# Kernel optimization log

Measured on AMD Instinct MI355X. Metric: run time of the kernel, lower is better.

Reference implementation:

```python
import jax, jax.numpy as jnp
import numpy as np

H = 4
D = 64          # attention_head_size
HID = H * D     # 256
LN_EPS = 1e-12


def setup_inputs() -> dict:
    key = jax.random.key(0)
    ks = jax.random.split(key, 20)
    B, S = 8, 200
    s = 0.02
    inp = {
        'input_tensor': jax.random.normal(ks[0], (B, S, HID), jnp.float32),
        'attention_mask': jnp.zeros((B, 1, S, S), jnp.float32),
        'absolute_pos_K': jax.random.normal(ks[1], (B, S, HID), jnp.float32),
        'absolute_pos_V': jax.random.normal(ks[2], (B, S, HID), jnp.float32),
        'time_matrix_emb_K': jax.random.normal(ks[3], (B, S, S, HID), jnp.float32),
        'time_matrix_emb_V': jax.random.normal(ks[4], (B, S, S, HID), jnp.float32),
        'Wq': jax.random.normal(ks[5], (HID, HID), jnp.float32) * s,
        'bq': jnp.zeros((HID,), jnp.float32),
        'Wk': jax.random.normal(ks[6], (HID, HID), jnp.float32) * s,
        'bk': jnp.zeros((HID,), jnp.float32),
        'Wv': jax.random.normal(ks[7], (HID, HID), jnp.float32) * s,
        'bv': jnp.zeros((HID,), jnp.float32),
        'order_w': jax.random.normal(ks[8], (2 * D,), jnp.float32) * s,
        'order_b': jnp.zeros((), jnp.float32),
        'dist_w': jax.random.normal(ks[9], (2 * D,), jnp.float32) * s,
        'dist_b': jnp.zeros((), jnp.float32),
        'scalar': jax.random.normal(ks[10], (1,), jnp.float32),
        'Wd': jax.random.normal(ks[11], (HID, HID), jnp.float32) * s,
        'bd': jnp.zeros((HID,), jnp.float32),
        'ln_g': jnp.ones((HID,), jnp.float32),
        'ln_b': jnp.zeros((HID,), jnp.float32),
    }
    return inp


def _forward(input_tensor, attention_mask, absolute_pos_K, absolute_pos_V,
             time_matrix_emb_K, time_matrix_emb_V,
             Wq, bq, Wk, bk, Wv, bv, order_w, order_b, dist_w, dist_b,
             scalar, Wd, bd, ln_g, ln_b):
    B, S, _ = input_tensor.shape
    heads = lambda x: x.reshape(B, S, H, D).transpose(0, 2, 1, 3)  # -> [B,H,S,D]
    q = heads(input_tensor @ Wq + bq)
    k = heads(input_tensor @ Wk + bk)
    v = heads(input_tensor @ Wv + bv)
    posK = heads(absolute_pos_K)                                   # [B,H,S,D]
    posV = heads(absolute_pos_V)
    timeK = time_matrix_emb_K.reshape(B, S, S, H, D).transpose(0, 3, 1, 2, 4)  # [B,H,S,S,D]
    timeV = time_matrix_emb_V.reshape(B, S, S, H, D).transpose(0, 3, 1, 2, 4)

    scores = (jnp.einsum('bhid,bhjd->bhij', q, k)
              + jnp.einsum('bhid,bhjd->bhij', q, posK)
              + jnp.einsum('bhijd,bhid->bhij', timeK, q))          # [B,H,S,S]

    # order_affine(cat(q_i,k_j)) == q_i@w[:D] + k_j@w[D:] + b (Linear on concat)
    pr_order = jax.nn.sigmoid(jnp.einsum('bhid,d->bhi', q, order_w[:D])[:, :, :, None]
                              + jnp.einsum('bhjd,d->bhj', k, order_w[D:])[:, :, None, :]
                              + order_b)
    gd_order = jnp.triu(jnp.ones((S, S), jnp.float32), 1)[None, None]
    error_order = (jnp.log(pr_order + 1e-24) * gd_order
                   + jnp.log(1.0 - pr_order + 1e-24) * (1.0 - gd_order))

    idx = jnp.arange(S, dtype=jnp.float32)
    gd_dist = jnp.log(jnp.abs(idx[None, :] - idx[:, None]) + 1.0)[None, None]
    pr_dist = (jnp.einsum('bhid,d->bhi', q, dist_w[:D])[:, :, :, None]
               + jnp.einsum('bhjd,d->bhj', k, dist_w[D:])[:, :, None, :]
               + dist_b)
    error_distance = -jnp.square(gd_dist - pr_dist) * jnp.square(scalar[0]) / 2.0

    scores = scores + error_order + error_distance
    probs = jax.nn.softmax(scores / np.sqrt(D) + attention_mask, axis=-1)

    ctx = (jnp.einsum('bhij,bhjd->bhid', probs, v)
           + jnp.einsum('bhij,bhjd->bhid', probs, posV)
           + jnp.einsum('bhij,bhijd->bhid', probs, timeV))
    ctx = ctx.transpose(0, 2, 1, 3).reshape(B, S, HID)

    hs = ctx @ Wd + bd + input_tensor
    mu = jnp.mean(hs, axis=-1, keepdims=True)
    var = jnp.mean(jnp.square(hs - mu), axis=-1, keepdims=True)
    return (hs - mu) / jnp.sqrt(var + LN_EPS) * ln_g + ln_b


def reference(input_tensor, attention_mask, absolute_pos_K, absolute_pos_V,
              time_matrix_emb_K, time_matrix_emb_V,
              Wq, bq, Wk, bk, Wv, bv, order_w, order_b, dist_w, dist_b,
              scalar, Wd, bd, ln_g, ln_b):
    return _forward(input_tensor, attention_mask, absolute_pos_K, absolute_pos_V,
                    time_matrix_emb_K, time_matrix_emb_V,
                    Wq, bq, Wk, bk, Wv, bv, order_w, order_b, dist_w, dist_b,
                    scalar, Wd, bd, ln_g, ln_b)
```

## Files before the change

kernel.cpp:

```cpp
#include <hip/hip_runtime.h>

#define SB 8
#define SS 200
#define HID 256
#define NH 4
#define DH 64

typedef float f32x4_t __attribute__((ext_vector_type(4)));

__device__ __forceinline__ float4 ntload4(const float* p) {
    f32x4_t v = __builtin_nontemporal_load((const f32x4_t*)p);
    return make_float4(v.x, v.y, v.z, v.w);
}

__global__ __launch_bounds__(256) void proj_fused_kernel(
    const float* __restrict__ in,
    const float* __restrict__ Wq, const float* __restrict__ bq,
    const float* __restrict__ Wk, const float* __restrict__ bk,
    const float* __restrict__ Wv, const float* __restrict__ bv,
    const float* __restrict__ posK, const float* __restrict__ posV,
    const float* __restrict__ order_w, const float* __restrict__ dist_w,
    float* __restrict__ q_out, float* __restrict__ kpk_out,
    float* __restrict__ vpv_out,
    float* __restrict__ qo, float* __restrict__ ko,
    float* __restrict__ qd, float* __restrict__ kd)
{
    const int which = blockIdx.y;
    const float* W = (which == 0) ? Wq : (which == 1) ? Wk : Wv;
    const float* bias = (which == 0) ? bq : (which == 1) ? bk : bv;
    const int row0 = blockIdx.x * 8;
    __shared__ float sin_[8][HID];
    const int t = threadIdx.x;
    #pragma unroll
    for (int r = 0; r < 8; r++)
        sin_[r][t] = in[(size_t)(row0 + r) * HID + t];
    __syncthreads();

    const int tx = t & 63, ty = t >> 6;
    const int c0 = tx * 4, r0 = ty * 2;
    float acc[2][4] = {};
    #pragma unroll 4
    for (int kk = 0; kk < HID; kk++) {
        const float4 wv4 = *(const float4*)(W + (size_t)kk * HID + c0);
        const float a0 = sin_[r0][kk];
        const float a1 = sin_[r0 + 1][kk];
        acc[0][0] += a0 * wv4.x; acc[0][1] += a0 * wv4.y;
        acc[0][2] += a0 * wv4.z; acc[0][3] += a0 * wv4.w;
        acc[1][0] += a1 * wv4.x; acc[1][1] += a1 * wv4.y;
        acc[1][2] += a1 * wv4.z; acc[1][3] += a1 * wv4.w;
    }

    const float4 b4 = *(const float4*)(bias + c0);
    const int hh = tx >> 4;
    const int dd4 = (tx & 15) * 4;
    float4 ow4 = make_float4(0.f, 0.f, 0.f, 0.f);
    float4 dw4 = make_float4(0.f, 0.f, 0.f, 0.f);
    if (which == 0) {
        ow4 = *(const float4*)(order_w + dd4);
        dw4 = *(const float4*)(dist_w + dd4);
    } else if (which == 1) {
        ow4 = *(const float4*)(order_w + 64 + dd4);
        dw4 = *(const float4*)(dist_w + 64 + dd4);
    }

    #pragma unroll
    for (int rr = 0; rr < 2; rr++) {
        const int row = row0 + r0 + rr;
        const size_t off = (size_t)row * HID + c0;
        float4 o;
        o.x = acc[rr][0] + b4.x;
        o.y = acc[rr][1] + b4.y;
        o.z = acc[rr][2] + b4.z;
        o.w = acc[rr][3] + b4.w;
        if (which == 0) {
            *(float4*)(q_out + off) = o;
            float po = o.x * ow4.x + o.y * ow4.y + o.z * ow4.z + o.w * ow4.w;
            float pd = o.x * dw4.x + o.y * dw4.y + o.z * dw4.z + o.w * dw4.w;
            #pragma unroll
            for (int m = 1; m <= 8; m <<= 1) {
                po += __shfl_xor(po, m, 64);
                pd += __shfl_xor(pd, m, 64);
            }
            if ((tx & 15) == 0) {
                qo[row * NH + hh] = po;
                qd[row * NH + hh] = pd;
            }
        } else if (which == 1) {
            const float4 p4 = *(const float4*)(posK + off);
            float4 s;
            s.x = o.x + p4.x; s.y = o.y + p4.y;
            s.z = o.z + p4.z; s.w = o.w + p4.w;
            *(float4*)(kpk_out + off) = s;
            float po = o.x * ow4.x + o.y * ow4.y + o.z * ow4.z + o.w * ow4.w;
            float pd = o.x * dw4.x + o.y * dw4.y + o.z * dw4.z + o.w * dw4.w;
            #pragma unroll
            for (int m = 1; m <= 8; m <<= 1) {
                po += __shfl_xor(po, m, 64);
                pd += __shfl_xor(pd, m, 64);
            }
            if ((tx & 15) == 0) {
                ko[row * NH + hh] = po;
                kd[row * NH + hh] = pd;
            }
        } else {
            const float4 p4 = *(const float4*)(posV + off);
            float4 s;
            s.x = o.x + p4.x; s.y = o.y + p4.y;
            s.z = o.z + p4.z; s.w = o.w + p4.w;
            *(float4*)(vpv_out + off) = s;
        }
    }
}

__global__ __launch_bounds__(256) void attn_fused_kernel(
    const float* __restrict__ q, const float* __restrict__ kpk,
    const float* __restrict__ vpv,
    const float* __restrict__ timeK, const float* __restrict__ timeV,
    const float* __restrict__ mask,
    const float* __restrict__ qo, const float* __restrict__ ko,
    const float* __restrict__ qd, const float* __restrict__ kd,
    const float* __restrict__ order_b_p, const float* __restrict__ dist_b_p,
    const float* __restrict__ scalar_p,
    const float* __restrict__ Wd, const float* __restrict__ bd,
    const float* __restrict__ input,
    const float* __restrict__ ln_g, const float* __restrict__ ln_b,
    float* __restrict__ out)
{
    const int blk = blockIdx.x;
    const int b = blk / SS, i = blk - b * SS;
    const int t = threadIdx.x;
    const int w = t >> 6, l = t & 63;
    const int h = l >> 4;
    const int sub = l & 15;

    __shared__ float sh_q[HID];
    __shared__ float sh_e[NH][SS + 8];
    __shared__ float sh_s[NH][SS + 8];
    __shared__ float sh_red[4][HID];
    __shared__ float sh_c[HID];
    __shared__ float red2[4];

    const size_t rowq = (size_t)blk * HID;
    sh_q[t] = q[rowq + t];

    const float order_b = *order_b_p;
    const float dist_b = *dist_b_p;
    const float sc = *scalar_p;
    const float sc2h = 0.5f * sc * sc;
    const size_t tb = (size_t)blk * SS;
    for (int idx = t; idx < NH * SS; idx += 256) {
        const int eh = idx & 3, j = idx >> 2;
        const float xo = qo[blk * NH + eh] + ko[(b * SS + j) * NH + eh] + order_b;
        const float pr = 1.0f / (1.0f + __expf(-xo));
        const float eo = (j > i) ? __logf(pr + 1e-24f) : __logf(1.0f - pr + 1e-24f);
        const float xd = qd[blk * NH + eh] + kd[(b * SS + j) * NH + eh] + dist_b;
        const float gd = __logf(fabsf((float)(i - j)) + 1.0f);
        const float dv = gd - xd;
        sh_e[eh][j] = (eo - dv * dv * sc2h) * 0.125f + mask[tb + j];
    }
    __syncthreads();

    const int d0 = l * 4;
    const float4 qr = *(const float4*)(sh_q + d0);

    for (int j0 = 0; j0 < SS; j0 += 8) {
        const int ja = j0 + w, jb = ja + 4;
        const float4 ta = ntload4(timeK + (tb + ja) * (size_t)HID + d0);
        const float4 tb4 = ntload4(timeK + (tb + jb) * (size_t)HID + d0);
        const float4 ka = *(const float4*)(kpk + ((size_t)(b * SS + ja)) * HID + d0);
        const float4 kb = *(const float4*)(kpk + ((size_t)(b * SS + jb)) * HID + d0);
        float pa = (ta.x + ka.x) * qr.x + (ta.y + ka.y) * qr.y
                 + (ta.z + ka.z) * qr.z + (ta.w + ka.w) * qr.w;
        float pb = (tb4.x + kb.x) * qr.x + (tb4.y + kb.y) * qr.y
                 + (tb4.z + kb.z) * qr.z + (tb4.w + kb.w) * qr.w;
        pa += __shfl_xor(pa, 1, 64); pb += __shfl_xor(pb, 1, 64);
        pa += __shfl_xor(pa, 2, 64); pb += __shfl_xor(pb, 2, 64);
        pa += __shfl_xor(pa, 4, 64); pb += __shfl_xor(pb, 4, 64);
        pa += __shfl_xor(pa, 8, 64); pb += __shfl_xor(pb, 8, 64);
        if (sub == 0) {
            sh_s[h][ja] = pa * 0.125f + sh_e[h][ja];
            sh_s[h][jb] = pb * 0.125f + sh_e[h][jb];
        }
    }
    __syncthreads();

    {
        float vals[4];
        float m = -1e30f;
        #pragma unroll
        for (int rep = 0; rep < 4; rep++) {
            const int j = l + rep * 64;
            vals[rep] = (j < SS) ? sh_s[w][j] : -1e30f;
            m = fmaxf(m, vals[rep]);
        }
        #pragma unroll
        for (int mm = 32; mm >= 1; mm >>= 1) m = fmaxf(m, __shfl_xor(m, mm, 64));
        float sum = 0.0f;
        float es[4];
        #pragma unroll
        for (int rep = 0; rep < 4; rep++) {
            const int j = l + rep * 64;
            if (j < SS) { es[rep] = __expf(vals[rep] - m); sum += es[rep]; }
        }
        #pragma unroll
        for (int mm = 32; mm >= 1; mm >>= 1) sum += __shfl_xor(sum, mm, 64);
        const float inv = 1.0f / sum;
        #pragma unroll
        for (int rep = 0; rep < 4; rep++) {
            const int j = l + rep * 64;
            if (j < SS) sh_s[w][j] = es[rep] * inv;
        }
    }
    __syncthreads();

    float4 acc = make_float4(0.f, 0.f, 0.f, 0.f);
    for (int j0 = 0; j0 < SS; j0 += 8) {
        const int ja = j0 + w, jb = ja + 4;
        const float4 ta = ntload4(timeV + (tb + ja) * (size_t)HID + d0);
        const float4 tb4 = ntload4(timeV + (tb + jb) * (size_t)HID + d0);
        const float4 va = *(const float4*)(vpv + ((size_t)(b * SS + ja)) * HID + d0);
        const float4 vb = *(const float4*)(vpv + ((size_t)(b * SS + jb)) * HID + d0);
        const float pa = sh_s[h][ja];
        const float pb = sh_s[h][jb];
        acc.x += pa * (ta.x + va.x) + pb * (tb4.x + vb.x);
        acc.y += pa * (ta.y + va.y) + pb * (tb4.y + vb.y);
        acc.z += pa * (ta.z + va.z) + pb * (tb4.z + vb.z);
        acc.w += pa * (ta.w + va.w) + pb * (tb4.w + vb.w);
    }
    *(float4*)(&sh_red[w][d0]) = acc;
    __syncthreads();
    sh_c[t] = sh_red[0][t] + sh_red[1][t] + sh_red[2][t] + sh_red[3][t];
    __syncthreads();

    float hsv = bd[t] + input[rowq + t];
    #pragma unroll 4
    for (int kk = 0; kk < HID; kk++)
        hsv += sh_c[kk] * Wd[(size_t)kk * HID + t];

    float s = hsv;
    #pragma unroll
    for (int m = 32; m >= 1; m >>= 1) s += __shfl_xor(s, m, 64);
    if (l == 0) red2[w] = s;
    __syncthreads();
    const float mu = (red2[0] + red2[1] + red2[2] + red2[3]) * (1.0f / 256.0f);
    __syncthreads();
    const float dv = hsv - mu;
    float s2 = dv * dv;
    #pragma unroll
    for (int m = 32; m >= 1; m >>= 1) s2 += __shfl_xor(s2, m, 64);
    if (l == 0) red2[w] = s2;
    __syncthreads();
    const float var = (red2[0] + red2[1] + red2[2] + red2[3]) * (1.0f / 256.0f);
    out[rowq + t] = dv * rsqrtf(var + 1e-12f) * ln_g[t] + ln_b[t];
}

extern "C" void kernel_launch(void* const* d_in, const int* in_sizes, int n_in,
                              void* d_out, int out_size, void* d_ws, size_t ws_size,
                              hipStream_t stream) {
    const float* input   = (const float*)d_in[0];
    const float* mask    = (const float*)d_in[1];
    const float* posK    = (const float*)d_in[2];
    const float* posV    = (const float*)d_in[3];
    const float* timeK   = (const float*)d_in[4];
    const float* timeV   = (const float*)d_in[5];
    const float* Wq      = (const float*)d_in[6];
    const float* bq      = (const float*)d_in[7];
    const float* Wk      = (const float*)d_in[8];
    const float* bk      = (const float*)d_in[9];
    const float* Wv      = (const float*)d_in[10];
    const float* bv      = (const float*)d_in[11];
    const float* order_w = (const float*)d_in[12];
    const float* order_b = (const float*)d_in[13];
    const float* dist_w  = (const float*)d_in[14];
    const float* dist_b  = (const float*)d_in[15];
    const float* scalar  = (const float*)d_in[16];
    const float* Wd      = (const float*)d_in[17];
    const float* bd      = (const float*)d_in[18];
    const float* ln_g    = (const float*)d_in[19];
    const float* ln_b    = (const float*)d_in[20];

    const int NROW = SB * SS;
    float* ws = (float*)d_ws;
    float* q_ws   = ws;
    float* kpk_ws = q_ws   + 409600;
    float* vpv_ws = kpk_ws + 409600;
    float* qo_ws  = vpv_ws + 409600;
    float* ko_ws  = qo_ws  + 6400;
    float* qd_ws  = ko_ws  + 6400;
    float* kd_ws  = qd_ws  + 6400;

    proj_fused_kernel<<<dim3(NROW / 8, 3), 256, 0, stream>>>(
        input, Wq, bq, Wk, bk, Wv, bv, posK, posV, order_w, dist_w,
        q_ws, kpk_ws, vpv_ws, qo_ws, ko_ws, qd_ws, kd_ws);
    attn_fused_kernel<<<NROW, 256, 0, stream>>>(
        q_ws, kpk_ws, vpv_ws, timeK, timeV, mask,
        qo_ws, ko_ws, qd_ws, kd_ws, order_b, dist_b, scalar,
        Wd, bd, input, ln_g, ln_b, (float*)d_out);
}
```

Measured before the change: 697.6 us.

## Unroll timeK/timeV streams, defer bias-term computation, split Wd GEMV across waves

The timeK and timeV loops now issue four rows per wave per iteration instead of two, giving more memory loads in flight on the bandwidth-bound streams. The order/distance bias computation moves after the timeK pass, with one head per wave, so the kernel starts streaming without a barrier first; the bias is added when the softmax reads the scores. The output dense projection is split across the four waves with float4 Wd loads and reduced through shared memory, replacing a 256-step serial loop per thread. In exchange it uses more registers, which could lower occupancy.

```diff
diff --git a/kernel.cpp b/kernel.cpp
--- a/kernel.cpp
+++ b/kernel.cpp
@@ -142,44 +142,83 @@
 
     const size_t rowq = (size_t)blk * HID;
     sh_q[t] = q[rowq + t];
-
-    const float order_b = *order_b_p;
-    const float dist_b = *dist_b_p;
-    const float sc = *scalar_p;
-    const float sc2h = 0.5f * sc * sc;
-    const size_t tb = (size_t)blk * SS;
-    for (int idx = t; idx < NH * SS; idx += 256) {
-        const int eh = idx & 3, j = idx >> 2;
-        const float xo = qo[blk * NH + eh] + ko[(b * SS + j) * NH + eh] + order_b;
-        const float pr = 1.0f / (1.0f + __expf(-xo));
-        const float eo = (j > i) ? __logf(pr + 1e-24f) : __logf(1.0f - pr + 1e-24f);
-        const float xd = qd[blk * NH + eh] + kd[(b * SS + j) * NH + eh] + dist_b;
-        const float gd = __logf(fabsf((float)(i - j)) + 1.0f);
-        const float dv = gd - xd;
-        sh_e[eh][j] = (eo - dv * dv * sc2h) * 0.125f + mask[tb + j];
-    }
     __syncthreads();
 
     const int d0 = l * 4;
     const float4 qr = *(const float4*)(sh_q + d0);
-
-    for (int j0 = 0; j0 < SS; j0 += 8) {
-        const int ja = j0 + w, jb = ja + 4;
-        const float4 ta = ntload4(timeK + (tb + ja) * (size_t)HID + d0);
-        const float4 tb4 = ntload4(timeK + (tb + jb) * (size_t)HID + d0);
-        const float4 ka = *(const float4*)(kpk + ((size_t)(b * SS + ja)) * HID + d0);
-        const float4 kb = *(const float4*)(kpk + ((size_t)(b * SS + jb)) * HID + d0);
-        float pa = (ta.x + ka.x) * qr.x + (ta.y + ka.y) * qr.y
-                 + (ta.z + ka.z) * qr.z + (ta.w + ka.w) * qr.w;
-        float pb = (tb4.x + kb.x) * qr.x + (tb4.y + kb.y) * qr.y
-                 + (tb4.z + kb.z) * qr.z + (tb4.w + kb.w) * qr.w;
-        pa += __shfl_xor(pa, 1, 64); pb += __shfl_xor(pb, 1, 64);
-        pa += __shfl_xor(pa, 2, 64); pb += __shfl_xor(pb, 2, 64);
-        pa += __shfl_xor(pa, 4, 64); pb += __shfl_xor(pb, 4, 64);
-        pa += __shfl_xor(pa, 8, 64); pb += __shfl_xor(pb, 8, 64);
+    const size_t tb = (size_t)blk * SS;
+    const float* __restrict__ kpkb = kpk + (size_t)b * SS * HID;
+    const float* __restrict__ vpvb = vpv + (size_t)b * SS * HID;
+
+    for (int j0 = 0; j0 < 192; j0 += 16) {
+        const int ja = j0 + w;
+        const float4 t0 = ntload4(timeK + (tb + ja)      * (size_t)HID + d0);
+        const float4 t1 = ntload4(timeK + (tb + ja + 4)  * (size_t)HID + d0);
+        const float4 t2 = ntload4(timeK + (tb + ja + 8)  * (size_t)HID + d0);
+        const float4 t3 = ntload4(timeK + (tb + ja + 12) * (size_t)HID + d0);
+        const float4 k0 = *(const float4*)(kpkb + (size_t)(ja)      * HID + d0);
+        const float4 k1 = *(const float4*)(kpkb + (size_t)(ja + 4)  * HID + d0);
+        const float4 k2 = *(const float4*)(kpkb + (size_t)(ja + 8)  * HID + d0);
+        const float4 k3 = *(const float4*)(kpkb + (size_t)(ja + 12) * HID + d0);
+        float p0 = (t0.x + k0.x) * qr.x + (t0.y + k0.y) * qr.y
+                 + (t0.z + k0.z) * qr.z + (t0.w + k0.w) * qr.w;
+        float p1 = (t1.x + k1.x) * qr.x + (t1.y + k1.y) * qr.y
+                 + (t1.z + k1.z) * qr.z + (t1.w + k1.w) * qr.w;
+        float p2 = (t2.x + k2.x) * qr.x + (t2.y + k2.y) * qr.y
+                 + (t2.z + k2.z) * qr.z + (t2.w + k2.w) * qr.w;
+        float p3 = (t3.x + k3.x) * qr.x + (t3.y + k3.y) * qr.y
+                 + (t3.z + k3.z) * qr.z + (t3.w + k3.w) * qr.w;
+        #pragma unroll
+        for (int m = 1; m <= 8; m <<= 1) {
+            p0 += __shfl_xor(p0, m, 64);
+            p1 += __shfl_xor(p1, m, 64);
+            p2 += __shfl_xor(p2, m, 64);
+            p3 += __shfl_xor(p3, m, 64);
+        }
         if (sub == 0) {
-            sh_s[h][ja] = pa * 0.125f + sh_e[h][ja];
-            sh_s[h][jb] = pb * 0.125f + sh_e[h][jb];
+            sh_s[h][ja]      = p0 * 0.125f;
+            sh_s[h][ja + 4]  = p1 * 0.125f;
+            sh_s[h][ja + 8]  = p2 * 0.125f;
+            sh_s[h][ja + 12] = p3 * 0.125f;
+        }
+    }
+    {
+        const int ja = 192 + w, jb = 196 + w;
+        const float4 t0 = ntload4(timeK + (tb + ja) * (size_t)HID + d0);
+        const float4 t1 = ntload4(timeK + (tb + jb) * (size_t)HID + d0);
+        const float4 k0 = *(const float4*)(kpkb + (size_t)ja * HID + d0);
+        const float4 k1 = *(const float4*)(kpkb + (size_t)jb * HID + d0);
+        float p0 = (t0.x + k0.x) * qr.x + (t0.y + k0.y) * qr.y
+                 + (t0.z + k0.z) * qr.z + (t0.w + k0.w) * qr.w;
+        float p1 = (t1.x + k1.x) * qr.x + (t1.y + k1.y) * qr.y
+                 + (t1.z + k1.z) * qr.z + (t1.w + k1.w) * qr.w;
+        #pragma unroll
+        for (int m = 1; m <= 8; m <<= 1) {
+            p0 += __shfl_xor(p0, m, 64);
+            p1 += __shfl_xor(p1, m, 64);
+        }
+        if (sub == 0) {
+            sh_s[h][ja] = p0 * 0.125f;
+            sh_s[h][jb] = p1 * 0.125f;
+        }
+    }
+
+    {
+        const float order_b = *order_b_p;
+        const float dist_b = *dist_b_p;
+        const float sc = *scalar_p;
+        const float sc2h = 0.5f * sc * sc;
+        const float qo_w = qo[blk * NH + w];
+        const float qd_w = qd[blk * NH + w];
+        for (int j = l; j < SS; j += 64) {
+            const float xo = qo_w + ko[(b * SS + j) * NH + w] + order_b;
+            const float pr = 1.0f / (1.0f + __expf(-xo));
+            const float eo = (j > i) ? __logf(pr + 1e-24f)
+                                     : __logf(1.0f - pr + 1e-24f);
+            const float xd = qd_w + kd[(b * SS + j) * NH + w] + dist_b;
+            const float gd = __logf(fabsf((float)(i - j)) + 1.0f);
+            const float dv = gd - xd;
+            sh_e[w][j] = (eo - dv * dv * sc2h) * 0.125f + mask[tb + j];
         }
     }
     __syncthreads();
@@ -190,7 +229,7 @@
         #pragma unroll
         for (int rep = 0; rep < 4; rep++) {
             const int j = l + rep * 64;
-            vals[rep] = (j < SS) ? sh_s[w][j] : -1e30f;
+            vals[rep] = (j < SS) ? (sh_s[w][j] + sh_e[w][j]) : -1e30f;
             m = fmaxf(m, vals[rep]);
         }
         #pragma unroll
@@ -214,28 +253,68 @@
     __syncthreads();
 
     float4 acc = make_float4(0.f, 0.f, 0.f, 0.f);
-    for (int j0 = 0; j0 < SS; j0 += 8) {
-        const int ja = j0 + w, jb = ja + 4;
-        const float4 ta = ntload4(timeV + (tb + ja) * (size_t)HID + d0);
-        const float4 tb4 = ntload4(timeV + (tb + jb) * (size_t)HID + d0);
-        const float4 va = *(const float4*)(vpv + ((size_t)(b * SS + ja)) * HID + d0);
-        const float4 vb = *(const float4*)(vpv + ((size_t)(b * SS + jb)) * HID + d0);
-        const float pa = sh_s[h][ja];
-        const float pb = sh_s[h][jb];
-        acc.x += pa * (ta.x + va.x) + pb * (tb4.x + vb.x);
-        acc.y += pa * (ta.y + va.y) + pb * (tb4.y + vb.y);
-        acc.z += pa * (ta.z + va.z) + pb * (tb4.z + vb.z);
-        acc.w += pa * (ta.w + va.w) + pb * (tb4.w + vb.w);
+    for (int j0 = 0; j0 < 192; j0 += 16) {
+        const int ja = j0 + w;
+        const float4 t0 = ntload4(timeV + (tb + ja)      * (size_t)HID + d0);
+        const float4 t1 = ntload4(timeV + (tb + ja + 4)  * (size_t)HID + d0);
+        const float4 t2 = ntload4(timeV + (tb + ja + 8)  * (size_t)HID + d0);
+        const float4 t3 = ntload4(timeV + (tb + ja + 12) * (size_t)HID + d0);
+        const float4 v0 = *(const float4*)(vpvb + (size_t)(ja)      * HID + d0);
+        const float4 v1 = *(const float4*)(vpvb + (size_t)(ja + 4)  * HID + d0);
+        const float4 v2 = *(const float4*)(vpvb + (size_t)(ja + 8)  * HID + d0);
+        const float4 v3 = *(const float4*)(vpvb + (size_t)(ja + 12) * HID + d0);
+        const float p0 = sh_s[h][ja];
+        const float p1 = sh_s[h][ja + 4];
+        const float p2 = sh_s[h][ja + 8];
+        const float p3 = sh_s[h][ja + 12];
+        acc.x += p0 * (t0.x + v0.x) + p1 * (t1.x + v1.x)
+               + p2 * (t2.x + v2.x) + p3 * (t3.x + v3.x);
+        acc.y += p0 * (t0.y + v0.y) + p1 * (t1.y + v1.y)
+               + p2 * (t2.y + v2.y) + p3 * (t3.y + v3.y);
+        acc.z += p0 * (t0.z + v0.z) + p1 * (t1.z + v1.z)
+               + p2 * (t2.z + v2.z) + p3 * (t3.z + v3.z);
+        acc.w += p0 * (t0.w + v0.w) + p1 * (t1.w + v1.w)
+               + p2 * (t2.w + v2.w) + p3 * (t3.w + v3.w);
+    }
+    {
+        const int ja = 192 + w, jb = 196 + w;
+        const float4 t0 = ntload4(timeV + (tb + ja) * (size_t)HID + d0);
+        const float4 t1 = ntload4(timeV + (tb + jb) * (size_t)HID + d0);
+        const float4 v0 = *(const float4*)(vpvb + (size_t)ja * HID + d0);
+        const float4 v1 = *(const float4*)(vpvb + (size_t)jb * HID + d0);
+        const float p0 = sh_s[h][ja];
+        const float p1 = sh_s[h][jb];
+        acc.x += p0 * (t0.x + v0.x) + p1 * (t1.x + v1.x);
+        acc.y += p0 * (t0.y + v0.y) + p1 * (t1.y + v1.y);
+        acc.z += p0 * (t0.z + v0.z) + p1 * (t1.z + v1.z);
+        acc.w += p0 * (t0.w + v0.w) + p1 * (t1.w + v1.w);
     }
     *(float4*)(&sh_red[w][d0]) = acc;
     __syncthreads();
     sh_c[t] = sh_red[0][t] + sh_red[1][t] + sh_red[2][t] + sh_red[3][t];
     __syncthreads();
 
-    float hsv = bd[t] + input[rowq + t];
-    #pragma unroll 4
-    for (int kk = 0; kk < HID; kk++)
-        hsv += sh_c[kk] * Wd[(size_t)kk * HID + t];
+    {
+        float4 a = make_float4(0.f, 0.f, 0.f, 0.f);
+        const int kbase = w * 64;
+        #pragma unroll 4
+        for (int kk = 0; kk < 64; kk += 4) {
+            const float4 c4 = *(const float4*)(sh_c + kbase + kk);
+            const float4 w0 = *(const float4*)(Wd + (size_t)(kbase + kk)     * HID + d0);
+            const float4 w1 = *(const float4*)(Wd + (size_t)(kbase + kk + 1) * HID + d0);
+            const float4 w2 = *(const float4*)(Wd + (size_t)(kbase + kk + 2) * HID + d0);
+            const float4 w3 = *(const float4*)(Wd + (size_t)(kbase + kk + 3) * HID + d0);
+            a.x += c4.x * w0.x + c4.y * w1.x + c4.z * w2.x + c4.w * w3.x;
+            a.y += c4.x * w0.y + c4.y * w1.y + c4.z * w2.y + c4.w * w3.y;
+            a.z += c4.x * w0.z + c4.y * w1.z + c4.z * w2.z + c4.w * w3.z;
+            a.w += c4.x * w0.w + c4.y * w1.w + c4.z * w2.w + c4.w * w3.w;
+        }
+        *(float4*)(&sh_red[w][d0]) = a;
+    }
+    __syncthreads();
+
+    const float hsv = sh_red[0][t] + sh_red[1][t] + sh_red[2][t] + sh_red[3][t]
+                    + bd[t] + input[rowq + t];
 
     float s = hsv;
     #pragma unroll
```

Measured after the change: 692.7 us. No clear change (-0.7%).
